# Kernel optimization log

Measured on AMD Instinct MI355X. Metric: run time of the kernel, lower is better.

Reference implementation:

```python
import jax, jax.numpy as jnp
import numpy as np

MARGIN = 0.3
EPS = 1e-6  # torch pairwise_distance eps inside triplet_margin_loss


def setup_inputs() -> dict:
    key = jax.random.key(0)
    k_e, k_l = jax.random.split(key)
    B, D, C = 8192, 128, 512
    emb = jax.random.normal(k_e, (B, D), dtype=jnp.float32)
    emb = emb / jnp.linalg.norm(emb, axis=-1, keepdims=True)  # docstring: L2-normalized
    labels = jax.random.randint(k_l, (B,), 0, C, dtype=jnp.int32)
    return {"embeddings": emb, "labels": labels}


def _pairwise_distances(emb):
    dot = emb @ emb.T                      # (B,B)
    sq = jnp.diagonal(dot)                 # (B,)
    d2 = sq[None, :] - 2.0 * dot + sq[:, None]
    return jnp.sqrt(jnp.clip(d2, 0.0))


def reference(embeddings, labels):
    B = embeddings.shape[0]
    # Mining uses distances only to produce indices -> no grad path in torch either.
    d = jax.lax.stop_gradient(_pairwise_distances(embeddings))

    same = labels[:, None] == labels[None, :]          # (B,B)
    eye = jnp.eye(B, dtype=bool)
    pos_mask = same & ~eye
    neg_mask = ~same
    valid = pos_mask.any(1) & neg_mask.any(1)           # anchors actually usable

    key = jax.random.key(42)
    kp, kn = jax.random.split(key)
    neg_inf = jnp.float32(-jnp.inf)

    # random positive per anchor via Gumbel-max over the positive mask
    gp = jax.random.gumbel(kp, (B, B), dtype=jnp.float32)
    pos_idx = jnp.argmax(jnp.where(pos_mask, gp, neg_inf), axis=1)   # (B,)
    ap = jnp.take_along_axis(d, pos_idx[:, None], axis=1)            # (B,1)

    # semi-hard negatives: ap < d(a,n) < ap + margin
    semi = neg_mask & (d > ap) & (d < ap + MARGIN)
    has_semi = semi.any(1)
    gn = jax.random.gumbel(kn, (B, B), dtype=jnp.float32)
    rand_semi = jnp.argmax(jnp.where(semi, gn, neg_inf), axis=1)
    hard_neg = jnp.argmin(jnp.where(neg_mask, d, jnp.inf), axis=1)   # fallback: hardest
    neg_idx = jnp.where(has_semi, rand_semi, hard_neg)

    a = embeddings
    p = embeddings[pos_idx]
    n = embeddings[neg_idx]
    dap = jnp.linalg.norm(a - p + EPS, axis=-1)
    dan = jnp.linalg.norm(a - n + EPS, axis=-1)
    per = jax.nn.relu(dap - dan + MARGIN)
    cnt = jnp.maximum(jnp.sum(valid.astype(jnp.float32)), 1.0)
    return jnp.sum(jnp.where(valid, per, 0.0)) / cnt
```

## Files before the change

kernel.cpp:

```cpp
#include <hip/hip_runtime.h>
#include <stdint.h>

#define B 8192
#define D 128
#define MARGIN 0.3f
#define EPS 1e-6f
#define HALFN (1u << 25)
#define NCHUNK 32
#define JCH (B / NCHUNK)
#define NPART 2048

using bf16x8 = __attribute__((ext_vector_type(8))) short;
using f32x16 = __attribute__((ext_vector_type(16))) float;
typedef unsigned long long u64;

__host__ __device__ __forceinline__ void tf2x32(uint32_t k0, uint32_t k1,
                                                uint32_t x0, uint32_t x1,
                                                uint32_t& o0, uint32_t& o1) {
  uint32_t ks2 = k0 ^ k1 ^ 0x1BD11BDAu;
  uint32_t v0 = x0 + k0, v1 = x1 + k1;
#define RND(r) { v0 += v1; v1 = (v1 << (r)) | (v1 >> (32 - (r))); v1 ^= v0; }
  RND(13) RND(15) RND(26) RND(6)
  v0 += k1;  v1 += ks2 + 1u;
  RND(17) RND(29) RND(16) RND(24)
  v0 += ks2; v1 += k0 + 2u;
  RND(13) RND(15) RND(26) RND(6)
  v0 += k0;  v1 += k1 + 3u;
  RND(17) RND(29) RND(16) RND(24)
  v0 += k1;  v1 += ks2 + 4u;
  RND(13) RND(15) RND(26) RND(6)
  v0 += ks2; v1 += k0 + 5u;
#undef RND
  o0 = v0; o1 = v1;
}

__device__ __forceinline__ uint32_t gbits(uint32_t k0, uint32_t k1, uint32_t f) {
  bool lo = f < HALFN;
  uint32_t x0 = lo ? f : f - HALFN;
  uint32_t x1 = lo ? f + HALFN : f;
  uint32_t o0, o1;
  tf2x32(k0, k1, x0, x1, o0, o1);
  return (lo ? o0 : o1) >> 9;
}

__device__ __forceinline__ uint16_t f2bf(float f) {
  uint32_t u = __float_as_uint(f);
  return (uint16_t)((u + 0x7FFFu + ((u >> 16) & 1u)) >> 16);
}
__device__ __forceinline__ float bf2f(uint16_t b) {
  return __uint_as_float((uint32_t)b << 16);
}
__device__ __forceinline__ bf16x8 as_bf(uint4 u) {
  union { uint4 a; bf16x8 b; } x; x.a = u; return x.b;
}

__global__ __launch_bounds__(256) void prep_kernel(const float* __restrict__ emb,
                                                   uint32_t* __restrict__ chunk,
                                                   float* __restrict__ sq,
                                                   u64* __restrict__ semikey,
                                                   u64* __restrict__ hardkey) {
  int tid = blockIdx.x * 256 + threadIdx.x;
  int row = tid >> 4, oct = tid & 15;
  const float* src = emb + row * D + oct * 8;
  uint32_t hi[4], lo[4];
  float s = 0.0f;
  #pragma unroll
  for (int e = 0; e < 4; e++) {
    float f0 = src[2 * e], f1 = src[2 * e + 1];
    s = fmaf(f0, f0, s); s = fmaf(f1, f1, s);
    uint16_t h0 = f2bf(f0), h1 = f2bf(f1);
    uint16_t l0 = f2bf(__fsub_rn(f0, bf2f(h0)));
    uint16_t l1 = f2bf(__fsub_rn(f1, bf2f(h1)));
    hi[e] = (uint32_t)h0 | ((uint32_t)h1 << 16);
    lo[e] = (uint32_t)l0 | ((uint32_t)l1 << 16);
  }
  s += __shfl_xor(s, 1); s += __shfl_xor(s, 2);
  s += __shfl_xor(s, 4); s += __shfl_xor(s, 8);
  if (oct == 0) { sq[row] = s; semikey[row] = 0ull; hardkey[row] = ~0ull; }
  int g = row >> 5, kk = oct >> 1, lane = ((oct & 1) << 5) | (row & 31);
  uint32_t base = ((g * 8 + kk) * 2) * 64 + lane;
  *(uint4*)&chunk[(size_t)base * 4]        = make_uint4(hi[0], hi[1], hi[2], hi[3]);
  *(uint4*)&chunk[(size_t)(base + 64) * 4] = make_uint4(lo[0], lo[1], lo[2], lo[3]);
}

__global__ __launch_bounds__(256) void pos_kernel(
    const float* __restrict__ emb, const int* __restrict__ labels,
    const float* __restrict__ sq, uint32_t kp0, uint32_t kp1,
    int* __restrict__ posx, float* __restrict__ ap2lo, float* __restrict__ ap2hi,
    int* __restrict__ validf) {
  __shared__ int s_cnt[4];
  __shared__ int s_list[4][80];
  int wid = threadIdx.x >> 6, lane = threadIdx.x & 63;
  int i = blockIdx.x * 4 + wid;
  int lab = labels[i];
  if (lane == 0) s_cnt[wid] = 0;
  __syncthreads();
  for (int it = 0; it < B / 256; it++) {
    int j0 = it * 256 + lane * 4;
    int4 lv = *(const int4*)&labels[j0];
    #pragma unroll
    for (int e = 0; e < 4; e++) {
      if ((&lv.x)[e] == lab) {
        int pp = atomicAdd(&s_cnt[wid], 1);
        if (pp < 80) s_list[wid][pp] = j0 + e;
      }
    }
  }
  __syncthreads();
  int cnt = s_cnt[wid];

  uint32_t fbase = (uint32_t)i << 13;
  uint32_t bb = 0; int bi = -1;
  for (int t = lane; t < cnt; t += 64) {
    int j = s_list[wid][t];
    if (j != i) {
      uint32_t bits = gbits(kp0, kp1, fbase | (uint32_t)j);
      if (bi < 0 || bits > bb || (bits == bb && j < bi)) { bb = bits; bi = j; }
    }
  }
  #pragma unroll
  for (int off = 32; off > 0; off >>= 1) {
    uint32_t ob = __shfl_xor(bb, off);
    int oi = __shfl_xor(bi, off);
    if (oi >= 0 && (bi < 0 || ob > bb || (ob == bb && oi < bi))) { bb = ob; bi = oi; }
  }
  int pidx = (cnt >= 2) ? bi : 0;

  float a0 = emb[i * D + lane],    a1 = emb[i * D + 64 + lane];
  float p0 = emb[pidx * D + lane], p1 = emb[pidx * D + 64 + lane];
  float dot = fmaf(a1, p1, a0 * p0);
  #pragma unroll
  for (int off = 32; off > 0; off >>= 1) dot += __shfl_xor(dot, off);

  if (lane == 0) {
    float d2 = __fadd_rn(__fsub_rn(sq[pidx], __fmul_rn(2.0f, dot)), sq[i]);
    float apv = __fsqrt_rn(fmaxf(d2, 0.0f));
    float apm = __fadd_rn(apv, MARGIN);
    ap2lo[i] = __fmul_rn(apv, apv);
    ap2hi[i] = __fmul_rn(apm, apm);
    posx[i] = pidx;
    validf[i] = (cnt >= 2 && cnt < B) ? 1 : 0;
  }
}

__global__ __launch_bounds__(256, 3) void main_kernel(
    const uint32_t* __restrict__ chunk, const int* __restrict__ labels,
    const float* __restrict__ sq, const float* __restrict__ ap2lo,
    const float* __restrict__ ap2hi, uint32_t kn0, uint32_t kn1,
    u64* __restrict__ semikey, u64* __restrict__ hardkey) {
  __shared__ uint32_t ldsB[8192];
  __shared__ int s_labj[64];
  __shared__ float s_sqj[64];

  const int tid = threadIdx.x;
  const int w = tid >> 6, lane = tid & 63;
  const int p = lane & 31, khalf = lane >> 5;
  const int A0 = blockIdx.x * 128;
  const int jc = blockIdx.y;
  const int ia_lo = A0 + 32 * w + p;
  const int ia_up = ia_lo + 4096;

  bf16x8 Af[2][8];
  {
    int g_lo = (A0 >> 5) + w;
    #pragma unroll
    for (int m = 0; m < 2; m++) {
      int g = g_lo + (m ? 128 : 0);
      #pragma unroll
      for (int kk = 0; kk < 8; kk++)
        Af[m][kk] = as_bf(*(const uint4*)&chunk[(size_t)(((g * 8 + kk) * 2) * 64 + lane) * 4]);
    }
  }

  const int lab_lo = labels[ia_lo], lab_up = labels[ia_up];
  const float sq_lo = sq[ia_lo], sq_up = sq[ia_up];
  const float tl2_lo = ap2lo[ia_lo], tl2_up = ap2lo[ia_up];
  const float th2_lo = ap2hi[ia_lo], th2_up = ap2hi[ia_up];
  const uint32_t fb = (uint32_t)ia_lo << 13;
  u64 sk_lo = 0ull, sk_up = 0ull;
  u64 hk_lo = ~0ull, hk_up = ~0ull;

  for (int jt = 0; jt < JCH; jt += 64) {
    const int jb = jc * JCH + jt;
    __syncthreads();
    {
      const uint32_t* src = chunk + (size_t)(jb >> 5) * 4096;
      #pragma unroll
      for (int q = 0; q < 8; q++) {
        int idx = tid + 256 * q;
        *(uint4*)&ldsB[idx * 4] = *(const uint4*)&src[idx * 4];
      }
      if (tid < 64) { s_labj[tid] = labels[jb + tid]; s_sqj[tid] = sq[jb + tid]; }
    }
    __syncthreads();

    #pragma unroll
    for (int n0 = 0; n0 < 2; n0++) {
      f32x16 acc[2];
      acc[0] = (f32x16)(0.0f);
      acc[1] = (f32x16)(0.0f);

      #pragma unroll
      for (int kk = 0; kk < 8; kk++) {
        bf16x8 jh = *(const bf16x8*)&ldsB[(size_t)((n0 * 16 + kk * 2 + 0) * 64 + lane) * 4];
        bf16x8 jl = *(const bf16x8*)&ldsB[(size_t)((n0 * 16 + kk * 2 + 1) * 64 + lane) * 4];
        acc[0] = __builtin_amdgcn_mfma_f32_32x32x16_bf16(jh, Af[0][kk], acc[0], 0, 0, 0);
        acc[0] = __builtin_amdgcn_mfma_f32_32x32x16_bf16(jl, Af[0][kk], acc[0], 0, 0, 0);
        acc[1] = __builtin_amdgcn_mfma_f32_32x32x16_bf16(jh, Af[1][kk], acc[1], 0, 0, 0);
        acc[1] = __builtin_amdgcn_mfma_f32_32x32x16_bf16(jl, Af[1][kk], acc[1], 0, 0, 0);
      }

      #pragma unroll
      for (int g = 0; g < 4; g++) {
        uint32_t blo[4], bup[4];
        #pragma unroll
        for (int t = 0; t < 4; t++) {
          int row = t + (g << 3) + (khalf << 2);
          uint32_t f = fb | (uint32_t)(jb + n0 * 32 + row);
          uint32_t o0, o1;
          tf2x32(kn0, kn1, f, f + HALFN, o0, o1);
          blo[t] = o0 >> 9; bup[t] = o1 >> 9;
        }
        #pragma unroll
        for (int t = 0; t < 4; t++) {
          int r = (g << 2) + t;
          int row = t + (g << 3) + (khalf << 2);
          int jl_ = n0 * 32 + row;
          int j = jb + jl_;
          float sj = s_sqj[jl_];
          int lj = s_labj[jl_];
          float d2lo = __fadd_rn(fmaf(-2.0f, acc[0][r], sj), sq_lo);
          float d2up = __fadd_rn(fmaf(-2.0f, acc[1][r], sj), sq_up);
          bool neg_lo = (lj != lab_lo), neg_up = (lj != lab_up);
          u64 rj = (u64)(8191 - j);
          u64 cs_lo = neg_lo && (d2lo > tl2_lo) && (d2lo < th2_lo)
                        ? ((((u64)blo[t] << 13) | rj) + 1ull) : 0ull;
          u64 cs_up = neg_up && (d2up > tl2_up) && (d2up < th2_up)
                        ? ((((u64)bup[t] << 13) | rj) + 1ull) : 0ull;
          if (cs_lo > sk_lo) sk_lo = cs_lo;
          if (cs_up > sk_up) sk_up = cs_up;
          u64 ch_lo = neg_lo ? (((u64)__float_as_uint(d2lo) << 13) | (u64)j) : ~0ull;
          u64 ch_up = neg_up ? (((u64)__float_as_uint(d2up) << 13) | (u64)j) : ~0ull;
          if (ch_lo < hk_lo) hk_lo = ch_lo;
          if (ch_up < hk_up) hk_up = ch_up;
        }
      }
    }
  }

  {
    u64 o;
    o = __shfl_xor(sk_lo, 32); if (o > sk_lo) sk_lo = o;
    o = __shfl_xor(sk_up, 32); if (o > sk_up) sk_up = o;
    o = __shfl_xor(hk_lo, 32); if (o < hk_lo) hk_lo = o;
    o = __shfl_xor(hk_up, 32); if (o < hk_up) hk_up = o;
  }
  if (lane < 32) {
    atomicMax(&semikey[ia_lo], sk_lo);
    atomicMin(&hardkey[ia_lo], hk_lo);
  } else {
    atomicMax(&semikey[ia_up], sk_up);
    atomicMin(&hardkey[ia_up], hk_up);
  }
}

__global__ __launch_bounds__(256) void finalize_kernel(
    const float* __restrict__ emb, const int* __restrict__ posx,
    const int* __restrict__ validf,
    const u64* __restrict__ semikey, const u64* __restrict__ hardkey,
    float* __restrict__ pers, float* __restrict__ cnts) {
  __shared__ float s_per[4];
  __shared__ float s_cnt[4];
  int wid = threadIdx.x >> 6, lane = threadIdx.x & 63;
  int i = blockIdx.x * 4 + wid;

  u64 sk = semikey[i];
  u64 hk = hardkey[i];
  int neg = sk ? (8191 - (int)((sk - 1ull) & 8191ull)) : (int)(hk & 8191ull);
  if (hk == ~0ull && !sk) neg = 0;
  int pos = posx[i];

  float sap = 0.0f, san = 0.0f;
  #pragma unroll
  for (int k = lane; k < D; k += 64) {
    float a = emb[i * D + k];
    float dp = __fadd_rn(__fsub_rn(a, emb[pos * D + k]), EPS);
    float dn = __fadd_rn(__fsub_rn(a, emb[neg * D + k]), EPS);
    sap = fmaf(dp, dp, sap);
    san = fmaf(dn, dn, san);
  }
  #pragma unroll
  for (int off = 32; off > 0; off >>= 1) {
    sap += __shfl_down(sap, off);
    san += __shfl_down(san, off);
  }
  if (lane == 0) {
    int v = validf[i];
    float per = __fadd_rn(__fsub_rn(__fsqrt_rn(sap), __fsqrt_rn(san)), MARGIN);
    per = fmaxf(per, 0.0f);
    s_per[wid] = v ? per : 0.0f;
    s_cnt[wid] = v ? 1.0f : 0.0f;
  }
  __syncthreads();
  if (threadIdx.x == 0) {
    pers[blockIdx.x] = s_per[0] + s_per[1] + s_per[2] + s_per[3];
    cnts[blockIdx.x] = s_cnt[0] + s_cnt[1] + s_cnt[2] + s_cnt[3];
  }
}

__global__ __launch_bounds__(256) void reduce_kernel(
    const float* __restrict__ pers, const float* __restrict__ cnts,
    float* __restrict__ out) {
  __shared__ float rp[256], rcn[256];
  int tid = threadIdx.x;
  float sp = 0.0f, sc = 0.0f;
  #pragma unroll
  for (int q = 0; q < NPART / 256; q++) {
    sp += pers[tid + 256 * q];
    sc += cnts[tid + 256 * q];
  }
  rp[tid] = sp; rcn[tid] = sc;
  __syncthreads();
  for (int s = 128; s > 0; s >>= 1) {
    if (tid < s) { rp[tid] += rp[tid + s]; rcn[tid] += rcn[tid + s]; }
    __syncthreads();
  }
  if (tid == 0) out[0] = rp[0] / fmaxf(rcn[0], 1.0f);
}

extern "C" void kernel_launch(void* const* d_in, const int* in_sizes, int n_in,
                              void* d_out, int out_size, void* d_ws, size_t ws_size,
                              hipStream_t stream) {
  const float* emb = (const float*)d_in[0];
  const int* labels = (const int*)d_in[1];
  char* ws = (char*)d_ws;
  float* sq      = (float*)(ws + 0);
  float* ap2lo   = (float*)(ws + 32768);
  float* ap2hi   = (float*)(ws + 65536);
  int* posx      = (int*)(ws + 98304);
  int* validf    = (int*)(ws + 131072);
  float* pers    = (float*)(ws + 163840);
  float* cnts    = (float*)(ws + 180224);
  u64* semikey   = (u64*)(ws + 196608);
  u64* hardkey   = (u64*)(ws + 262144);
  uint32_t* chnk = (uint32_t*)(ws + 327680);
  float* out     = (float*)d_out;

  uint32_t A0, B0, A1, B1;
  tf2x32(0u, 42u, 0u, 2u, A0, B0);
  tf2x32(0u, 42u, 1u, 3u, A1, B1);
  uint32_t kp0 = A0, kp1 = A1, kn0 = B0, kn1 = B1;

  prep_kernel<<<512, 256, 0, stream>>>(emb, chnk, sq, semikey, hardkey);
  pos_kernel<<<B / 4, 256, 0, stream>>>(emb, labels, sq, kp0, kp1, posx, ap2lo, ap2hi, validf);
  main_kernel<<<dim3(32, NCHUNK), 256, 0, stream>>>(chnk, labels, sq, ap2lo, ap2hi,
                                                    kn0, kn1, semikey, hardkey);
  finalize_kernel<<<NPART, 256, 0, stream>>>(emb, posx, validf, semikey, hardkey,
                                             pers, cnts);
  reduce_kernel<<<1, 256, 0, stream>>>(pers, cnts, out);
}
```

Baseline: 186.7 us.

## Pack mining keys into 32-bit and simplify per-element threshold math

Switches the semi-hard and hardest-negative argmax/argmin keys from 64-bit to 32-bit. The semi key uses fewer Gumbel bits and the hard key uses a truncated distance mantissa. It folds the anchor squared norm and the key-add of Threefry into precomputed constants, and shifts distances by +4 so they stay positive for the unsigned compare. It also raises main_kernel occupancy to 4 blocks per SM, aiming to cut the integer ALU and register cost of the 64-bit compares in the inner loop. The truncation risks changing which element is chosen when keys tie, so the result may differ from the reference.

```diff
diff --git a/kernel.cpp b/kernel.cpp
--- a/kernel.cpp
+++ b/kernel.cpp
@@ -12,7 +12,6 @@
 
 using bf16x8 = __attribute__((ext_vector_type(8))) short;
 using f32x16 = __attribute__((ext_vector_type(16))) float;
-typedef unsigned long long u64;
 
 __host__ __device__ __forceinline__ void tf2x32(uint32_t k0, uint32_t k1,
                                                 uint32_t x0, uint32_t x1,
@@ -34,6 +33,25 @@
   o0 = v0; o1 = v1;
 }
 
+__device__ __forceinline__ void tf_rounds(uint32_t k0, uint32_t k1,
+                                          uint32_t v0, uint32_t v1,
+                                          uint32_t& o0, uint32_t& o1) {
+  uint32_t ks2 = k0 ^ k1 ^ 0x1BD11BDAu;
+#define RNDL(r) { v0 += v1; v1 = __builtin_rotateleft32(v1, r); v1 ^= v0; }
+  RNDL(13) RNDL(15) RNDL(26) RNDL(6)
+  v0 += k1;  v1 += ks2 + 1u;
+  RNDL(17) RNDL(29) RNDL(16) RNDL(24)
+  v0 += ks2; v1 += k0 + 2u;
+  RNDL(13) RNDL(15) RNDL(26) RNDL(6)
+  v0 += k0;  v1 += k1 + 3u;
+  RNDL(17) RNDL(29) RNDL(16) RNDL(24)
+  v0 += k1;  v1 += ks2 + 4u;
+  RNDL(13) RNDL(15) RNDL(26) RNDL(6)
+  v0 += ks2; v1 += k0 + 5u;
+#undef RNDL
+  o0 = v0; o1 = v1;
+}
+
 __device__ __forceinline__ uint32_t gbits(uint32_t k0, uint32_t k1, uint32_t f) {
   bool lo = f < HALFN;
   uint32_t x0 = lo ? f : f - HALFN;
@@ -57,8 +75,8 @@
 __global__ __launch_bounds__(256) void prep_kernel(const float* __restrict__ emb,
                                                    uint32_t* __restrict__ chunk,
                                                    float* __restrict__ sq,
-                                                   u64* __restrict__ semikey,
-                                                   u64* __restrict__ hardkey) {
+                                                   uint32_t* __restrict__ semikey,
+                                                   uint32_t* __restrict__ hardkey) {
   int tid = blockIdx.x * 256 + threadIdx.x;
   int row = tid >> 4, oct = tid & 15;
   const float* src = emb + row * D + oct * 8;
@@ -76,7 +94,7 @@
   }
   s += __shfl_xor(s, 1); s += __shfl_xor(s, 2);
   s += __shfl_xor(s, 4); s += __shfl_xor(s, 8);
-  if (oct == 0) { sq[row] = s; semikey[row] = 0ull; hardkey[row] = ~0ull; }
+  if (oct == 0) { sq[row] = s; semikey[row] = 0u; hardkey[row] = 0xFFFFFFFFu; }
   int g = row >> 5, kk = oct >> 1, lane = ((oct & 1) << 5) | (row & 31);
   uint32_t base = ((g * 8 + kk) * 2) * 64 + lane;
   *(uint4*)&chunk[(size_t)base * 4]        = make_uint4(hi[0], hi[1], hi[2], hi[3]);
@@ -143,14 +161,14 @@
   }
 }
 
-__global__ __launch_bounds__(256, 3) void main_kernel(
+__global__ __launch_bounds__(256, 4) void main_kernel(
     const uint32_t* __restrict__ chunk, const int* __restrict__ labels,
     const float* __restrict__ sq, const float* __restrict__ ap2lo,
     const float* __restrict__ ap2hi, uint32_t kn0, uint32_t kn1,
-    u64* __restrict__ semikey, u64* __restrict__ hardkey) {
+    uint32_t* __restrict__ semikey, uint32_t* __restrict__ hardkey) {
   __shared__ uint32_t ldsB[8192];
   __shared__ int s_labj[64];
-  __shared__ float s_sqj[64];
+  __shared__ float s_sqj4[64];
 
   const int tid = threadIdx.x;
   const int w = tid >> 6, lane = tid & 63;
@@ -174,11 +192,14 @@
 
   const int lab_lo = labels[ia_lo], lab_up = labels[ia_up];
   const float sq_lo = sq[ia_lo], sq_up = sq[ia_up];
-  const float tl2_lo = ap2lo[ia_lo], tl2_up = ap2lo[ia_up];
-  const float th2_lo = ap2hi[ia_lo], th2_up = ap2hi[ia_up];
-  const uint32_t fb = (uint32_t)ia_lo << 13;
-  u64 sk_lo = 0ull, sk_up = 0ull;
-  u64 hk_lo = ~0ull, hk_up = ~0ull;
+  const float Xlo_lo = __fadd_rn(__fsub_rn(ap2lo[ia_lo], sq_lo), 4.0f);
+  const float Xhi_lo = __fadd_rn(__fsub_rn(ap2hi[ia_lo], sq_lo), 4.0f);
+  const float Xlo_up = __fadd_rn(__fsub_rn(ap2lo[ia_up], sq_up), 4.0f);
+  const float Xhi_up = __fadd_rn(__fsub_rn(ap2hi[ia_up], sq_up), 4.0f);
+  const uint32_t c0 = ((uint32_t)ia_lo << 13) + kn0;
+  const uint32_t c1 = ((uint32_t)ia_lo << 13) + HALFN + kn1;
+  uint32_t sk_lo = 0u, sk_up = 0u;
+  uint32_t hk_lo = 0xFFFFFFFFu, hk_up = 0xFFFFFFFFu;
 
   for (int jt = 0; jt < JCH; jt += 64) {
     const int jb = jc * JCH + jt;
@@ -190,7 +211,7 @@
         int idx = tid + 256 * q;
         *(uint4*)&ldsB[idx * 4] = *(const uint4*)&src[idx * 4];
       }
-      if (tid < 64) { s_labj[tid] = labels[jb + tid]; s_sqj[tid] = sq[jb + tid]; }
+      if (tid < 64) { s_labj[tid] = labels[jb + tid]; s_sqj4[tid] = sq[jb + tid] + 4.0f; }
     }
     __syncthreads();
 
@@ -216,10 +237,10 @@
         #pragma unroll
         for (int t = 0; t < 4; t++) {
           int row = t + (g << 3) + (khalf << 2);
-          uint32_t f = fb | (uint32_t)(jb + n0 * 32 + row);
+          uint32_t jv = (uint32_t)(jb + n0 * 32 + row);
           uint32_t o0, o1;
-          tf2x32(kn0, kn1, f, f + HALFN, o0, o1);
-          blo[t] = o0 >> 9; bup[t] = o1 >> 9;
+          tf_rounds(kn0, kn1, c0 + jv, c1 + jv, o0, o1);
+          blo[t] = o0 >> 13; bup[t] = o1 >> 13;
         }
         #pragma unroll
         for (int t = 0; t < 4; t++) {
@@ -227,33 +248,35 @@
           int row = t + (g << 3) + (khalf << 2);
           int jl_ = n0 * 32 + row;
           int j = jb + jl_;
-          float sj = s_sqj[jl_];
+          float sj4 = s_sqj4[jl_];
           int lj = s_labj[jl_];
-          float d2lo = __fadd_rn(fmaf(-2.0f, acc[0][r], sj), sq_lo);
-          float d2up = __fadd_rn(fmaf(-2.0f, acc[1][r], sj), sq_up);
-          bool neg_lo = (lj != lab_lo), neg_up = (lj != lab_up);
-          u64 rj = (u64)(8191 - j);
-          u64 cs_lo = neg_lo && (d2lo > tl2_lo) && (d2lo < th2_lo)
-                        ? ((((u64)blo[t] << 13) | rj) + 1ull) : 0ull;
-          u64 cs_up = neg_up && (d2up > tl2_up) && (d2up < th2_up)
-                        ? ((((u64)bup[t] << 13) | rj) + 1ull) : 0ull;
-          if (cs_lo > sk_lo) sk_lo = cs_lo;
-          if (cs_up > sk_up) sk_up = cs_up;
-          u64 ch_lo = neg_lo ? (((u64)__float_as_uint(d2lo) << 13) | (u64)j) : ~0ull;
-          u64 ch_up = neg_up ? (((u64)__float_as_uint(d2up) << 13) | (u64)j) : ~0ull;
-          if (ch_lo < hk_lo) hk_lo = ch_lo;
-          if (ch_up < hk_up) hk_up = ch_up;
+          float Xl = fmaf(-2.0f, acc[0][r], sj4);
+          float Xu = fmaf(-2.0f, acc[1][r], sj4);
+          bool nl = (lj != lab_lo), nu = (lj != lab_up);
+          uint32_t rj = (uint32_t)(8191 - j);
+          uint32_t keyl = (blo[t] << 13) | rj;
+          uint32_t keyu = (bup[t] << 13) | rj;
+          bool il = nl && (Xl > Xlo_lo) && (Xl < Xhi_lo);
+          bool iu = nu && (Xu > Xlo_up) && (Xu < Xhi_up);
+          uint32_t csl = il ? keyl : 0u;
+          uint32_t csu = iu ? keyu : 0u;
+          sk_lo = max(sk_lo, csl);
+          sk_up = max(sk_up, csu);
+          uint32_t hl = nl ? ((__float_as_uint(Xl) & 0xFFFFE000u) | (uint32_t)j) : 0xFFFFFFFFu;
+          uint32_t hu = nu ? ((__float_as_uint(Xu) & 0xFFFFE000u) | (uint32_t)j) : 0xFFFFFFFFu;
+          hk_lo = min(hk_lo, hl);
+          hk_up = min(hk_up, hu);
         }
       }
     }
   }
 
   {
-    u64 o;
-    o = __shfl_xor(sk_lo, 32); if (o > sk_lo) sk_lo = o;
-    o = __shfl_xor(sk_up, 32); if (o > sk_up) sk_up = o;
-    o = __shfl_xor(hk_lo, 32); if (o < hk_lo) hk_lo = o;
-    o = __shfl_xor(hk_up, 32); if (o < hk_up) hk_up = o;
+    uint32_t o;
+    o = __shfl_xor(sk_lo, 32); sk_lo = max(sk_lo, o);
+    o = __shfl_xor(sk_up, 32); sk_up = max(sk_up, o);
+    o = __shfl_xor(hk_lo, 32); hk_lo = min(hk_lo, o);
+    o = __shfl_xor(hk_up, 32); hk_up = min(hk_up, o);
   }
   if (lane < 32) {
     atomicMax(&semikey[ia_lo], sk_lo);
@@ -267,17 +290,17 @@
 __global__ __launch_bounds__(256) void finalize_kernel(
     const float* __restrict__ emb, const int* __restrict__ posx,
     const int* __restrict__ validf,
-    const u64* __restrict__ semikey, const u64* __restrict__ hardkey,
+    const uint32_t* __restrict__ semikey, const uint32_t* __restrict__ hardkey,
     float* __restrict__ pers, float* __restrict__ cnts) {
   __shared__ float s_per[4];
   __shared__ float s_cnt[4];
   int wid = threadIdx.x >> 6, lane = threadIdx.x & 63;
   int i = blockIdx.x * 4 + wid;
 
-  u64 sk = semikey[i];
-  u64 hk = hardkey[i];
-  int neg = sk ? (8191 - (int)((sk - 1ull) & 8191ull)) : (int)(hk & 8191ull);
-  if (hk == ~0ull && !sk) neg = 0;
+  uint32_t sk = semikey[i];
+  uint32_t hk = hardkey[i];
+  int neg = sk ? (8191 - (int)(sk & 8191u)) : (int)(hk & 8191u);
+  if (!sk && hk == 0xFFFFFFFFu) neg = 0;
   int pos = posx[i];
 
   float sap = 0.0f, san = 0.0f;
@@ -334,17 +357,17 @@
   const float* emb = (const float*)d_in[0];
   const int* labels = (const int*)d_in[1];
   char* ws = (char*)d_ws;
-  float* sq      = (float*)(ws + 0);
-  float* ap2lo   = (float*)(ws + 32768);
-  float* ap2hi   = (float*)(ws + 65536);
-  int* posx      = (int*)(ws + 98304);
-  int* validf    = (int*)(ws + 131072);
-  float* pers    = (float*)(ws + 163840);
-  float* cnts    = (float*)(ws + 180224);
-  u64* semikey   = (u64*)(ws + 196608);
-  u64* hardkey   = (u64*)(ws + 262144);
-  uint32_t* chnk = (uint32_t*)(ws + 327680);
-  float* out     = (float*)d_out;
+  float* sq        = (float*)(ws + 0);
+  float* ap2lo     = (float*)(ws + 32768);
+  float* ap2hi     = (float*)(ws + 65536);
+  int* posx        = (int*)(ws + 98304);
+  int* validf      = (int*)(ws + 131072);
+  float* pers      = (float*)(ws + 163840);
+  float* cnts      = (float*)(ws + 180224);
+  uint32_t* semikey= (uint32_t*)(ws + 196608);
+  uint32_t* hardkey= (uint32_t*)(ws + 229376);
+  uint32_t* chnk   = (uint32_t*)(ws + 262144);
+  float* out       = (float*)d_out;
 
   uint32_t A0, B0, A1, B1;
   tf2x32(0u, 42u, 0u, 2u, A0, B0);
```

Result: slower. 203.5 us (+9.0%).
